# Performance work log

Measured on AMD Instinct MI355X. Metric: run time of the kernel, lower is better.

The kernel has to match this reference:

```python
import jax, jax.numpy as jnp
import numpy as np

B, S, D, H = 32, 577, 768, 12
d = D // H  # dim per head
MLP = 4 * D
EPS = 1e-5


def setup_inputs() -> dict:
    key = jax.random.key(0)
    ks = jax.random.split(key, 6)
    sc = 0.02
    return {
        "x": jax.random.normal(ks[0], (B, S, D), jnp.float32),
        "ln1_g": jnp.ones((D,), jnp.float32),
        "ln1_b": jnp.zeros((D,), jnp.float32),
        "Wq": jax.random.normal(ks[1], (H, d, d), jnp.float32) * sc,
        "bq": jnp.zeros((H, d), jnp.float32),
        "Wk": jax.random.normal(ks[2], (H, d, d), jnp.float32) * sc,
        "bk": jnp.zeros((H, d), jnp.float32),
        "Wv": jax.random.normal(ks[3], (H, d, d), jnp.float32) * sc,
        "bv": jnp.zeros((H, d), jnp.float32),
        "ln2_g": jnp.ones((D,), jnp.float32),
        "ln2_b": jnp.zeros((D,), jnp.float32),
        "W1": jax.random.normal(ks[4], (D, MLP), jnp.float32) * sc,
        "b1": jnp.zeros((MLP,), jnp.float32),
        "W2": jax.random.normal(ks[5], (MLP, D), jnp.float32) * sc,
        "b2": jnp.zeros((D,), jnp.float32),
    }


def layer_norm(x, g, b):
    mu = jnp.mean(x, axis=-1, keepdims=True)
    var = jnp.mean(jnp.square(x - mu), axis=-1, keepdims=True)
    return (x - mu) * jax.lax.rsqrt(var + EPS) * g + b


def msa(x, Wq, bq, Wk, bk, Wv, bv):
    # x: [B,S,D]; each head only sees its own slice of the hidden dim.
    xh = x.reshape(B, S, H, d)
    q = jnp.einsum("bshd,hde->bshe", xh, Wq) + bq
    k = jnp.einsum("bshd,hde->bshe", xh, Wk) + bk
    v = jnp.einsum("bshd,hde->bshe", xh, Wv) + bv
    scores = jnp.einsum("bqhe,bkhe->bhqk", q, k) / jnp.sqrt(jnp.float32(d))
    attn = jax.nn.softmax(scores, axis=-1)  # [B,H,S,S]
    out = jnp.einsum("bhqk,bkhe->bqhe", attn, v)
    return out.reshape(B, S, D)  # head-wise hstack == reshape


def reference(x, ln1_g, ln1_b, Wq, bq, Wk, bk, Wv, bv, ln2_g, ln2_b, W1, b1, W2, b2):
    out = x + msa(layer_norm(x, ln1_g, ln1_b), Wq, bq, Wk, bk, Wv, bv)
    h = layer_norm(out, ln2_g, ln2_b)
    mlp = jax.nn.gelu(h @ W1 + b1, approximate=False) @ W2 + b2
    return out + mlp
```

## Files before the change

### kernel.cpp

```cpp
#include <hip/hip_runtime.h>
#include <hip/hip_bf16.h>


#define kB   32
#define kS   577
#define kD   768
#define kH   12
#define kd   64
#define kMLP 3072
#define kTOK (kB * kS)
#define kMPAD 18688

typedef short short8 __attribute__((ext_vector_type(8)));
typedef short short4v __attribute__((ext_vector_type(4)));
typedef float f32x4 __attribute__((ext_vector_type(4)));
typedef float f32x16 __attribute__((ext_vector_type(16)));
typedef unsigned u32x4 __attribute__((ext_vector_type(4)));
typedef __bf16 bf16x8 __attribute__((ext_vector_type(8)));

__device__ inline short f2bf(float f) {
  unsigned u = __float_as_uint(f);
  unsigned r = (u + 0x7FFFu + ((u >> 16) & 1u)) >> 16;
  return (short)r;
}

__device__ inline f32x4 mfma16(short8 a, short8 b, f32x4 c) {
  return __builtin_amdgcn_mfma_f32_16x16x32_bf16(
      __builtin_bit_cast(bf16x8, a), __builtin_bit_cast(bf16x8, b), c, 0, 0, 0);
}

__device__ inline f32x16 mfma32(short8 a, short8 b, f32x16 c) {
  return __builtin_amdgcn_mfma_f32_32x32x16_bf16(
      __builtin_bit_cast(bf16x8, a), __builtin_bit_cast(bf16x8, b), c, 0, 0, 0);
}

__device__ inline void load_lds16(const short* g, short* l) {
  __builtin_amdgcn_global_load_lds(
      (__attribute__((address_space(1))) void*)(g),
      (__attribute__((address_space(3))) void*)(l), 16, 0, 0);
}

__device__ inline unsigned cvtpk(float lo, float hi) {
  unsigned r;
  asm("v_cvt_pk_bf16_f32 %0, %1, %2" : "=v"(r) : "v"(lo), "v"(hi));
  return r;
}

__device__ inline void pl32(unsigned &a, unsigned &b) {
  typedef int int2v __attribute__((ext_vector_type(2)));
  int2v r = __builtin_amdgcn_permlane32_swap((int)a, (int)b, false, false);
  a = (unsigned)r[0];
  b = (unsigned)r[1];
}

__device__ inline float gelu_f(float x) {
  float u = x * x;
  float z = x * fmaf(0.0713548162f, u, 1.5957691216f);
  float e = __expf(z);
  return x - x / (e + 1.0f);
}

__global__ __launch_bounds__(256) void ln_kernel(const float* __restrict__ x,
                                                 const float* __restrict__ g,
                                                 const float* __restrict__ b,
                                                 short* __restrict__ out) {
  int row = blockIdx.x;
  const float* xr = x + (size_t)row * kD;
  int t = threadIdx.x;
  float v0 = xr[t], v1 = xr[t + 256], v2 = xr[t + 512];
  float s = v0 + v1 + v2;
  float ss = v0 * v0 + v1 * v1 + v2 * v2;
#pragma unroll
  for (int off = 1; off < 64; off <<= 1) {
    s += __shfl_xor(s, off, 64);
    ss += __shfl_xor(ss, off, 64);
  }
  __shared__ float red[8];
  int wid = t >> 6;
  if ((t & 63) == 0) { red[wid * 2] = s; red[wid * 2 + 1] = ss; }
  __syncthreads();
  s = red[0] + red[2] + red[4] + red[6];
  ss = red[1] + red[3] + red[5] + red[7];
  float mean = s * (1.f / kD);
  float var = ss * (1.f / kD) - mean * mean;
  float rstd = rsqrtf(var + 1e-5f);
  size_t o = (size_t)row * kD;
  out[o + t]       = f2bf((v0 - mean) * rstd * g[t]       + b[t]);
  out[o + t + 256] = f2bf((v1 - mean) * rstd * g[t + 256] + b[t + 256]);
  out[o + t + 512] = f2bf((v2 - mean) * rstd * g[t + 512] + b[t + 512]);
}

__global__ __launch_bounds__(256) void transpose_bf16(const float* __restrict__ in,
                                                      short* __restrict__ out,
                                                      int R, int C) {
  __shared__ short tile[64][66];
  int c0 = blockIdx.x * 64, r0 = blockIdx.y * 64;
  int t = threadIdx.x;
  int c = t & 63, rr = t >> 6;
#pragma unroll
  for (int p = 0; p < 16; p++) {
    int r = p * 4 + rr;
    tile[r][c] = f2bf(in[(size_t)(r0 + r) * C + c0 + c]);
  }
  __syncthreads();
  int r2 = t & 63, cc = t >> 6;
#pragma unroll
  for (int p = 0; p < 16; p++) {
    int c2 = p * 4 + cc;
    out[(size_t)(c0 + c2) * R + r0 + r2] = tile[r2][c2];
  }
}

__global__ void pack_qkv(const float* __restrict__ Wq, const float* __restrict__ Wk,
                         const float* __restrict__ Wv, short* __restrict__ out) {
  int idx = blockIdx.x * 256 + threadIdx.x;
  if (idx >= kH * 192 * kd) return;
  int h = idx / (192 * kd);
  int j = (idx / kd) % 192;
  int k = idx % kd;
  int m = j >> 6, e = j & 63;
  const float* W = (m == 0) ? Wq : (m == 1) ? Wk : Wv;
  out[idx] = f2bf(W[((size_t)h * kd + k) * kd + e]);
}

__global__ __launch_bounds__(192) void qkv_gemm(const short* __restrict__ xn,
                                                const short* __restrict__ wt,
                                                const float* __restrict__ bq,
                                                const float* __restrict__ bk,
                                                const float* __restrict__ bv,
                                                short* __restrict__ Qb,
                                                short* __restrict__ Kb,
                                                short* __restrict__ Vb) {
  int t0 = blockIdx.x * 64;
  int h = blockIdx.y;
  __shared__ __align__(16) short As[64][72];
  __shared__ __align__(16) short Bs[192][72];
  int tid = threadIdx.x;
  for (int c = tid; c < 64 * 8; c += 192) {
    int row = c >> 3, c8 = c & 7;
    short8 v = {};
    int tok = t0 + row;
    if (tok < kTOK) v = *(const short8*)(xn + (size_t)tok * kD + h * kd + c8 * 8);
    *(short8*)&As[row][c8 * 8] = v;
  }
  const short* wth = wt + (size_t)h * 192 * kd;
  for (int c = tid; c < 192 * 8; c += 192) {
    int row = c >> 3, c8 = c & 7;
    *(short8*)&Bs[row][c8 * 8] = *(const short8*)(wth + row * kd + c8 * 8);
  }
  __syncthreads();
  int w = tid >> 6, l = tid & 63, l15 = l & 15, l4 = l >> 4;
  f32x4 acc[4][4] = {};
  short8 aF[4][2], bF[4][2];
#pragma unroll
  for (int rf = 0; rf < 4; rf++)
#pragma unroll
    for (int kk = 0; kk < 2; kk++)
      aF[rf][kk] = *(const short8*)&As[16 * rf + l15][32 * kk + 8 * l4];
#pragma unroll
  for (int cf = 0; cf < 4; cf++)
#pragma unroll
    for (int kk = 0; kk < 2; kk++)
      bF[cf][kk] = *(const short8*)&Bs[w * 64 + 16 * cf + l15][32 * kk + 8 * l4];
#pragma unroll
  for (int rf = 0; rf < 4; rf++)
#pragma unroll
    for (int cf = 0; cf < 4; cf++) {
      f32x4 c = acc[rf][cf];
      c = mfma16(aF[rf][0], bF[cf][0], c);
      c = mfma16(aF[rf][1], bF[cf][1], c);
      acc[rf][cf] = c;
    }
  const float* bias = (w == 0) ? bq : (w == 1) ? bk : bv;
  short* Out = (w == 0) ? Qb : (w == 1) ? Kb : Vb;
  float scale = (w == 0) ? 0.125f : 1.0f;
#pragma unroll
  for (int rf = 0; rf < 4; rf++) {
    int rowb = 16 * rf + 4 * l4;
#pragma unroll
    for (int cf = 0; cf < 4; cf++) {
      int col = 16 * cf + l15;
      float bs = bias[h * kd + col];
#pragma unroll
      for (int r = 0; r < 4; r++) {
        int tok = t0 + rowb + r;
        if (tok >= kTOK) continue;
        int bb = tok / kS, ssi = tok % kS;
        Out[(((size_t)bb * kH + h) * kS + ssi) * kd + col] =
            f2bf((acc[rf][cf][r] + bs) * scale);
      }
    }
  }
}

__global__ __launch_bounds__(256) void attn_kernel(const short* __restrict__ Qb,
                                                   const short* __restrict__ Kb,
                                                   const short* __restrict__ Vb,
                                                   const float* __restrict__ x,
                                                   float* __restrict__ out) {
  int qt = blockIdx.x, h = blockIdx.y, b = blockIdx.z;
  const size_t baseHS = ((size_t)b * kH + h) * kS;
  __shared__ __align__(16) short Klds[2][64 * 64];
  __shared__ __align__(16) short Vlds[2][64 * 64];
  int tid = threadIdx.x;
  int w = tid >> 6, l = tid & 63;
  int l31 = l & 31, hi = l >> 5;
  int q0w = qt * 128 + w * 32;
  bool active = (q0w < kS);

  int qg = q0w + l31;
  const short* qp = Qb + (baseHS + (qg > 576 ? 576 : qg)) * kd + 8 * hi;
  short8 qf[4];
#pragma unroll
  for (int ks = 0; ks < 4; ks++) qf[ks] = *(const short8*)(qp + 16 * ks);

  auto stageK = [&](int kbase, short* dst) {
#pragma unroll
    for (int c = 0; c < 2; c++) {
      int chunk = tid + 256 * c;
      int row = chunk >> 3, sl = chunk & 7;
      int sr = kbase + row; if (sr > 576) sr = 576;
      load_lds16(Kb + (baseHS + sr) * kd + 8 * (sl ^ (row & 7)),
                 dst + (chunk & ~63) * 8);
    }
  };
  short4v vr0[2], vr1[2];
  auto stageV_load = [&](int kbase) {
#pragma unroll
    for (int c = 0; c < 2; c++) {
      int task = tid + 256 * c;
      int vp = task >> 4, vc = task & 15;
      int r0 = kbase + 2 * vp;     if (r0 > 576) r0 = 576;
      int r1 = kbase + 2 * vp + 1; if (r1 > 576) r1 = 576;
      vr0[c] = *(const short4v*)(Vb + (baseHS + r0) * kd + 4 * vc);
      vr1[c] = *(const short4v*)(Vb + (baseHS + r1) * kd + 4 * vc);
    }
  };
  auto stageV_write = [&](short* dst) {
#pragma unroll
    for (int c = 0; c < 2; c++) {
      int task = tid + 256 * c;
      int vp = task >> 4, vc = task & 15;
      int kv2 = 2 * vp;
#pragma unroll
      for (int j = 0; j < 4; j++) {
        int d = 4 * vc + j;
        *(unsigned*)((char*)dst + d * 128 + ((kv2 * 2) ^ ((d & 7) << 4))) =
            (unsigned)(unsigned short)vr0[c][j] |
            ((unsigned)(unsigned short)vr1[c][j] << 16);
      }
    }
  };

  stageK(0, Klds[0]);
  stageV_load(0);
  stageV_write(Vlds[0]);
  __syncthreads();

  f32x16 o0 = {}, o1 = {};
  float m_run = -1e30f, l_run = 0.f;
  int cur = 0;
  const int NT = 10;

  for (int kt = 0; kt < NT; kt++) {
    int kbase = kt * 64;
    bool has_next = (kt + 1 < NT);
    if (has_next) {
      stageK(kbase + 64, Klds[cur ^ 1]);
      stageV_load(kbase + 64);
    }
    u32x4 pa[4];
    if (active) {
      const char* Kc = (const char*)Klds[cur];
      f32x16 st0 = {}, st1 = {};
      __builtin_amdgcn_s_setprio(1);
#pragma unroll
      for (int ks = 0; ks < 4; ks++) {
        int xr = ((2 * ks + hi) ^ (l31 & 7)) << 4;
        short8 k0 = *(const short8*)(Kc + l31 * 128 + xr);
        short8 k1 = *(const short8*)(Kc + (32 + l31) * 128 + xr);
        st0 = mfma32(k0, qf[ks], st0);
        st1 = mfma32(k1, qf[ks], st1);
      }
      __builtin_amdgcn_s_setprio(0);
      if (kbase + 64 > kS) {
#pragma unroll
        for (int r = 0; r < 16; r++) {
          int cr = (r & 3) + 8 * (r >> 2) + 4 * hi;
          if (kbase + cr > 576)      st0[r] = -1e30f;
          if (kbase + 32 + cr > 576) st1[r] = -1e30f;
        }
      }
      float mx = st0[0];
#pragma unroll
      for (int r = 0; r < 16; r++) {
        mx = fmaxf(mx, st0[r]);
        mx = fmaxf(mx, st1[r]);
      }
      mx = fmaxf(mx, __shfl_xor(mx, 32, 64));
      bool need = !__all(mx <= m_run + 8.0f);
      if (need) {
        float mnew = fmaxf(m_run, mx);
        float al = __expf(m_run - mnew);
        m_run = mnew;
        l_run *= al;
#pragma unroll
        for (int r = 0; r < 16; r++) {
          int cr = (r & 3) + 8 * (r >> 2) + 4 * hi;
          float ar = __shfl(al, cr, 64);
          o0[r] *= ar;
          o1[r] *= ar;
        }
      }
      float rs = 0.f;
#pragma unroll
      for (int r = 0; r < 16; r++) {
        float p0 = __expf(st0[r] - m_run); st0[r] = p0;
        float p1 = __expf(st1[r] - m_run); st1[r] = p1;
        rs += p0 + p1;
      }
      rs += __shfl_xor(rs, 32, 64);
      l_run += rs;
      {
        unsigned a0 = cvtpk(st0[0], st0[1]),   b0 = cvtpk(st0[4], st0[5]);   pl32(a0, b0);
        unsigned a1 = cvtpk(st0[2], st0[3]),   b1 = cvtpk(st0[6], st0[7]);   pl32(a1, b1);
        pa[0] = (u32x4){a0, a1, b0, b1};
        unsigned c0 = cvtpk(st0[8], st0[9]),   d0 = cvtpk(st0[12], st0[13]); pl32(c0, d0);
        unsigned c1 = cvtpk(st0[10], st0[11]), d1 = cvtpk(st0[14], st0[15]); pl32(c1, d1);
        pa[1] = (u32x4){c0, c1, d0, d1};
        unsigned e0 = cvtpk(st1[0], st1[1]),   f0 = cvtpk(st1[4], st1[5]);   pl32(e0, f0);
        unsigned e1 = cvtpk(st1[2], st1[3]),   f1 = cvtpk(st1[6], st1[7]);   pl32(e1, f1);
        pa[2] = (u32x4){e0, e1, f0, f1};
        unsigned g0 = cvtpk(st1[8], st1[9]),   h0 = cvtpk(st1[12], st1[13]); pl32(g0, h0);
        unsigned g1 = cvtpk(st1[10], st1[11]), h1 = cvtpk(st1[14], st1[15]); pl32(g1, h1);
        pa[3] = (u32x4){g0, g1, h0, h1};
      }
      const char* Vc = (const char*)Vlds[cur];
      __builtin_amdgcn_s_setprio(1);
#pragma unroll
      for (int ks = 0; ks < 4; ks++) {
        int xr = ((2 * ks + hi) ^ (l31 & 7)) << 4;
        short8 v0 = *(const short8*)(Vc + l31 * 128 + xr);
        short8 v1 = *(const short8*)(Vc + (32 + l31) * 128 + xr);
        o0 = mfma32(__builtin_bit_cast(short8, pa[ks]), v0, o0);
        o1 = mfma32(__builtin_bit_cast(short8, pa[ks]), v1, o1);
      }
      __builtin_amdgcn_s_setprio(0);
    }
    if (has_next) stageV_write(Vlds[cur ^ 1]);
    __syncthreads();
    cur ^= 1;
  }

  if (active) {
#pragma unroll
    for (int r = 0; r < 16; r++) {
      int cr = (r & 3) + 8 * (r >> 2) + 4 * hi;
      int qq = q0w + cr;
      if (qq < kS) {
        float lq = __shfl(l_run, cr, 64);
        float rl = 1.0f / lq;
        size_t gi = ((size_t)b * kS + qq) * kD + h * kd + l31;
        out[gi]      = x[gi]      + o0[r] * rl;
        out[gi + 32] = x[gi + 32] + o1[r] * rl;
      } else {
        (void)__shfl(l_run, cr, 64);
      }
    }
  }
}

__global__ __launch_bounds__(512, 4) void gemm_bb(const short* __restrict__ A,
                                                  const short* __restrict__ BT,
                                                  const float* __restrict__ bias,
                                                  short* __restrict__ outb,
                                                  float* __restrict__ outf,
                                                  int M, int N, int K, int mode) {
  __shared__ __align__(16) short As[256 * 64];
  __shared__ __align__(16) short Bs[128 * 64];

  int nwg = gridDim.x, bid = blockIdx.x;
  int q = nwg >> 3, r = nwg & 7;
  int xcd = bid & 7, lx = bid >> 3;
  int swz = (xcd < r ? xcd * (q + 1) : r * (q + 1) + (xcd - r) * q) + lx;
  int gn = N >> 7;
  int nt = swz % gn, mt = swz / gn;
  int m0 = mt << 8, n0 = nt << 7;

  int tid = threadIdx.x;
  int w = tid >> 6, l = tid & 63, l15 = l & 15, l4 = l >> 4;
  int wm = w >> 1, wn = w & 1;

  int srow = tid >> 3;
  int sslot = (tid & 7) ^ (srow & 7);
  int sdst = (tid & ~63) * 8;
  const short* Asrc = A + (size_t)(m0 + srow) * K + sslot * 8;
  const short* Bsrc = BT + (size_t)(n0 + srow) * K + sslot * 8;

  const char* ldsA = (const char*)As + wm * 8192;
  const char* ldsB = (const char*)Bs + wn * 8192;

  f32x4 acc[4][4] = {};

  for (int k0 = 0; k0 < K; k0 += 64) {
    __syncthreads();
#pragma unroll
    for (int i = 0; i < 4; i++)
      load_lds16(Asrc + (size_t)(64 * i) * K + k0, As + i * 4096 + sdst);
#pragma unroll
    for (int j = 0; j < 2; j++)
      load_lds16(Bsrc + (size_t)(64 * j) * K + k0, Bs + j * 4096 + sdst);
    __syncthreads();
#pragma unroll
    for (int kk = 0; kk < 2; kk++) {
      short8 aF[4], bF[4];
#pragma unroll
      for (int i = 0; i < 4; i++) {
        int ra = 16 * i + l15;
        aF[i] = *(const short8*)(ldsA + ra * 128 + (((kk * 4 + l4) ^ (ra & 7)) << 4));
        bF[i] = *(const short8*)(ldsB + ra * 128 + (((kk * 4 + l4) ^ (ra & 7)) << 4));
      }
#pragma unroll
      for (int i = 0; i < 4; i++)
#pragma unroll
        for (int j = 0; j < 4; j++)
          acc[i][j] = mfma16(aF[i], bF[j], acc[i][j]);
    }
  }

#pragma unroll
  for (int i = 0; i < 4; i++) {
#pragma unroll
    for (int j = 0; j < 4; j++) {
      int col = n0 + wn * 64 + 16 * j + l15;
      float bs = bias[col];
#pragma unroll
      for (int rr = 0; rr < 4; rr++) {
        int row = m0 + wm * 64 + 16 * i + 4 * l4 + rr;
        if (row >= M) continue;
        float v = acc[i][j][rr] + bs;
        if (mode == 0) {
          outb[(size_t)row * N + col] = f2bf(gelu_f(v));
        } else {
          outf[(size_t)row * N + col] += v;
        }
      }
    }
  }
}

__global__ __launch_bounds__(256, 4) void gemm2b(const short* __restrict__ A,
                                                 const short* __restrict__ BT,
                                                 const float* __restrict__ bias,
                                                 float* __restrict__ outf,
                                                 int M, int N, int K) {
  __shared__ __align__(16) short As[128 * 64];
  __shared__ __align__(16) short Bs[128 * 64];

  int nwg = gridDim.x, bid = blockIdx.x;
  int q = nwg >> 3, r = nwg & 7;
  int xcd = bid & 7, lx = bid >> 3;
  int swz = (xcd < r ? xcd * (q + 1) : r * (q + 1) + (xcd - r) * q) + lx;
  int gn = N >> 7;
  int nt = swz % gn, mt = swz / gn;
  int m0 = mt << 7, n0 = nt << 7;

  int tid = threadIdx.x;
  int w = tid >> 6, l = tid & 63, l15 = l & 15, l4 = l >> 4;
  int wm = w >> 1, wn = w & 1;

  int srow = tid >> 3;
  int sslot = (tid & 7) ^ (srow & 7);
  int sdst = (tid & ~63) * 8;
  const short* Asrc = A + (size_t)(m0 + srow) * K + sslot * 8;
  const short* Bsrc = BT + (size_t)(n0 + srow) * K + sslot * 8;

  const char* ldsA = (const char*)As + wm * 8192;
  const char* ldsB = (const char*)Bs + wn * 8192;

  f32x4 acc[4][4] = {};

  for (int k0 = 0; k0 < K; k0 += 64) {
    __syncthreads();
#pragma unroll
    for (int i = 0; i < 4; i++)
      load_lds16(Asrc + (size_t)(32 * i) * K + k0, As + i * 2048 + sdst);
#pragma unroll
    for (int j = 0; j < 4; j++)
      load_lds16(Bsrc + (size_t)(32 * j) * K + k0, Bs + j * 2048 + sdst);
    __syncthreads();
#pragma unroll
    for (int kk = 0; kk < 2; kk++) {
      short8 aF[4], bF[4];
#pragma unroll
      for (int i = 0; i < 4; i++) {
        int ra = 16 * i + l15;
        aF[i] = *(const short8*)(ldsA + ra * 128 + (((kk * 4 + l4) ^ (ra & 7)) << 4));
        bF[i] = *(const short8*)(ldsB + ra * 128 + (((kk * 4 + l4) ^ (ra & 7)) << 4));
      }
#pragma unroll
      for (int i = 0; i < 4; i++)
#pragma unroll
        for (int j = 0; j < 4; j++)
          acc[i][j] = mfma16(aF[i], bF[j], acc[i][j]);
    }
  }

#pragma unroll
  for (int i = 0; i < 4; i++) {
#pragma unroll
    for (int j = 0; j < 4; j++) {
      int col = n0 + wn * 64 + 16 * j + l15;
      float bs = bias[col];
#pragma unroll
      for (int rr = 0; rr < 4; rr++) {
        int row = m0 + wm * 64 + 16 * i + 4 * l4 + rr;
        if (row >= M) continue;
        outf[(size_t)row * N + col] += acc[i][j][rr] + bs;
      }
    }
  }
}

extern "C" void kernel_launch(void* const* d_in, const int* in_sizes, int n_in,
                              void* d_out, int out_size, void* d_ws, size_t ws_size,
                              hipStream_t stream) {
  const float* x     = (const float*)d_in[0];
  const float* ln1_g = (const float*)d_in[1];
  const float* ln1_b = (const float*)d_in[2];
  const float* Wq    = (const float*)d_in[3];
  const float* bq    = (const float*)d_in[4];
  const float* Wk    = (const float*)d_in[5];
  const float* bk    = (const float*)d_in[6];
  const float* Wv    = (const float*)d_in[7];
  const float* bv    = (const float*)d_in[8];
  const float* ln2_g = (const float*)d_in[9];
  const float* ln2_b = (const float*)d_in[10];
  const float* W1    = (const float*)d_in[11];
  const float* b1    = (const float*)d_in[12];
  const float* W2    = (const float*)d_in[13];
  const float* b2    = (const float*)d_in[14];
  float* out = (float*)d_out;

  char* ws = (char*)d_ws;
  size_t off = 0;
  auto alloc = [&](size_t bytes) {
    size_t o = off;
    off += (bytes + 255) & ~(size_t)255;
    return o;
  };
  short* xn    = (short*)(ws + alloc((size_t)kTOK * kD * 2));
  short* wqkvT = (short*)(ws + alloc((size_t)kH * 192 * kd * 2));
  short* w1T   = (short*)(ws + alloc((size_t)kMLP * kD * 2));
  short* w2T   = (short*)(ws + alloc((size_t)kD * kMLP * 2));
  short* Qb    = (short*)(ws + alloc((size_t)kTOK * kD * 2));
  short* Kb    = (short*)(ws + alloc((size_t)kTOK * kD * 2));
  short* Vb    = (short*)(ws + alloc((size_t)kTOK * kD * 2));
  short* hbuf  = (short*)(ws + alloc((size_t)kMPAD * kD * 2));
  short* gbuf  = (short*)(ws + alloc((size_t)kMPAD * kMLP * 2));

  ln_kernel<<<kTOK, 256, 0, stream>>>(x, ln1_g, ln1_b, xn);
  transpose_bf16<<<dim3(kMLP / 64, kD / 64), 256, 0, stream>>>(W1, w1T, kD, kMLP);
  transpose_bf16<<<dim3(kD / 64, kMLP / 64), 256, 0, stream>>>(W2, w2T, kMLP, kD);
  pack_qkv<<<(kH * 192 * kd + 255) / 256, 256, 0, stream>>>(Wq, Wk, Wv, wqkvT);
  qkv_gemm<<<dim3((kTOK + 63) / 64, kH), 192, 0, stream>>>(xn, wqkvT, bq, bk, bv, Qb, Kb, Vb);
  attn_kernel<<<dim3(5, kH, kB), 256, 0, stream>>>(Qb, Kb, Vb, x, out);
  ln_kernel<<<kTOK, 256, 0, stream>>>(out, ln2_g, ln2_b, hbuf);
  gemm_bb<<<(kMPAD / 256) * (kMLP / 128), 512, 0, stream>>>(
      hbuf, w1T, b1, gbuf, nullptr, kTOK, kMLP, kD, 0);
  gemm2b<<<(kMPAD / 128) * (kD / 128), 256, 0, stream>>>(
      gbuf, w2T, b2, out, kTOK, kD, kMLP);
}
```

Measured before the change: 468.0 us.

## Double-buffer LDS in second MLP GEMM to overlap loads with MFMA

Converts the W2 GEMM kernel to a two-stage LDS ping-pong: the next K-tile is issued into the alternate buffer before computing the current one, with vmcnt waits and explicit barriers. It also raises wave priority around the MFMA block. The aim is to hide global-to-LDS latency behind matrix math. LDS per block doubles to 64KB, which may cut occupancy below the 4 blocks per CU the launch bounds request.

New measurement: 509.2 us. 1.09x slower.

```diff
diff --git a/kernel.cpp b/kernel.cpp
--- a/kernel.cpp
+++ b/kernel.cpp
@@ -449,13 +449,13 @@
   }
 }
 
-__global__ __launch_bounds__(256, 4) void gemm2b(const short* __restrict__ A,
+__global__ __launch_bounds__(256, 4) void gemm2p(const short* __restrict__ A,
                                                  const short* __restrict__ BT,
                                                  const float* __restrict__ bias,
                                                  float* __restrict__ outf,
                                                  int M, int N, int K) {
-  __shared__ __align__(16) short As[128 * 64];
-  __shared__ __align__(16) short Bs[128 * 64];
+  __shared__ __align__(16) short As[2][128 * 64];
+  __shared__ __align__(16) short Bs[2][128 * 64];
 
   int nwg = gridDim.x, bid = blockIdx.x;
   int q = nwg >> 3, r = nwg & 7;
@@ -475,20 +475,33 @@
   const short* Asrc = A + (size_t)(m0 + srow) * K + sslot * 8;
   const short* Bsrc = BT + (size_t)(n0 + srow) * K + sslot * 8;
 
-  const char* ldsA = (const char*)As + wm * 8192;
-  const char* ldsB = (const char*)Bs + wn * 8192;
+  auto stage = [&](int buf, int k0) {
+#pragma unroll
+    for (int i = 0; i < 4; i++)
+      load_lds16(Asrc + (size_t)(32 * i) * K + k0, &As[buf][i * 2048 + sdst]);
+#pragma unroll
+    for (int j = 0; j < 4; j++)
+      load_lds16(Bsrc + (size_t)(32 * j) * K + k0, &Bs[buf][j * 2048 + sdst]);
+  };
 
   f32x4 acc[4][4] = {};
-
-  for (int k0 = 0; k0 < K; k0 += 64) {
-    __syncthreads();
-#pragma unroll
-    for (int i = 0; i < 4; i++)
-      load_lds16(Asrc + (size_t)(32 * i) * K + k0, As + i * 2048 + sdst);
-#pragma unroll
-    for (int j = 0; j < 4; j++)
-      load_lds16(Bsrc + (size_t)(32 * j) * K + k0, Bs + j * 2048 + sdst);
-    __syncthreads();
+  int NT = K >> 6;
+
+  stage(0, 0);
+  for (int t = 0; t < NT; t++) {
+    int cur = t & 1;
+    if (t + 1 < NT) {
+      stage(cur ^ 1, (t + 1) << 6);
+      asm volatile("s_waitcnt vmcnt(8)" ::: "memory");
+    } else {
+      asm volatile("s_waitcnt vmcnt(0)" ::: "memory");
+    }
+    __builtin_amdgcn_sched_barrier(0);
+    __builtin_amdgcn_s_barrier();
+    __builtin_amdgcn_sched_barrier(0);
+
+    const char* ldsA = (const char*)&As[cur][0] + wm * 8192;
+    const char* ldsB = (const char*)&Bs[cur][0] + wn * 8192;
 #pragma unroll
     for (int kk = 0; kk < 2; kk++) {
       short8 aF[4], bF[4];
@@ -498,12 +511,17 @@
         aF[i] = *(const short8*)(ldsA + ra * 128 + (((kk * 4 + l4) ^ (ra & 7)) << 4));
         bF[i] = *(const short8*)(ldsB + ra * 128 + (((kk * 4 + l4) ^ (ra & 7)) << 4));
       }
+      __builtin_amdgcn_s_setprio(1);
 #pragma unroll
       for (int i = 0; i < 4; i++)
 #pragma unroll
         for (int j = 0; j < 4; j++)
           acc[i][j] = mfma16(aF[i], bF[j], acc[i][j]);
-    }
+      __builtin_amdgcn_s_setprio(0);
+    }
+    __builtin_amdgcn_sched_barrier(0);
+    __builtin_amdgcn_s_barrier();
+    __builtin_amdgcn_sched_barrier(0);
   }
 
 #pragma unroll
@@ -568,6 +586,6 @@
   ln_kernel<<<kTOK, 256, 0, stream>>>(out, ln2_g, ln2_b, hbuf);
   gemm_bb<<<(kMPAD / 256) * (kMLP / 128), 512, 0, stream>>>(
       hbuf, w1T, b1, gbuf, nullptr, kTOK, kMLP, kD, 0);
-  gemm2b<<<(kMPAD / 128) * (kD / 128), 256, 0, stream>>>(
+  gemm2p<<<(kMPAD / 128) * (kD / 128), 256, 0, stream>>>(
       gbuf, w2T, b2, out, kTOK, kD, kMLP);
 }
```
